# Performance work log

Hardware: AMD Instinct MI355X
Metric: run time of the kernel (lower is better)

The kernel has to match this reference:

```python
import jax, jax.numpy as jnp
import numpy as np

DIM = 128
HEADS = 4
K = 7          # neighborhood kernel size
MLP_RATIO = 4
EPS = 1e-5


def setup_inputs() -> dict:
    key = jax.random.key(0)
    ks = jax.random.split(key, 8)
    B, H, W, C = 4, 64, 64, DIM
    hid = C * MLP_RATIO
    s = lambda k, shape: jax.random.normal(k, shape, jnp.float32) * 0.02
    return {
        "x": jax.random.normal(ks[0], (B, H, W, C), jnp.float32),
        "ln1_g": jnp.ones((C,), jnp.float32),
        "ln1_b": jnp.zeros((C,), jnp.float32),
        "qkv_w": s(ks[1], (C, 3 * C)),
        "qkv_b": jnp.zeros((3 * C,), jnp.float32),
        "rpb": s(ks[2], (HEADS, 2 * K - 1, 2 * K - 1)),
        "proj_w": s(ks[3], (C, C)),
        "proj_b": jnp.zeros((C,), jnp.float32),
        "ln2_g": jnp.ones((C,), jnp.float32),
        "ln2_b": jnp.zeros((C,), jnp.float32),
        "fc1_w": s(ks[4], (C, hid)),
        "fc1_b": jnp.zeros((hid,), jnp.float32),
        "fc2_w": s(ks[5], (hid, C)),
        "fc2_b": jnp.zeros((C,), jnp.float32),
    }


def _ln(x, g, b):
    m = jnp.mean(x, axis=-1, keepdims=True)
    v = jnp.mean(jnp.square(x - m), axis=-1, keepdims=True)
    return (x - m) * jax.lax.rsqrt(v + EPS) * g + b


def _neigh_idx(L, k):
    # NATTEN border-clamped neighborhood: start = clamp(i - k//2, 0, L-k)
    i = jnp.arange(L)
    start = jnp.clip(i - k // 2, 0, L - k)
    idx = start[:, None] + jnp.arange(k)[None, :]        # [L, k] key positions
    rel = idx - i[:, None] + (k - 1)                     # [L, k] rpb indices in [0, 2k-2]
    return idx, rel


def _neighborhood_attention(x, qkv_w, qkv_b, rpb, proj_w, proj_b):
    B, H, W, C = x.shape
    nh, hd = HEADS, C // HEADS
    scale = hd ** -0.5
    qkv = (x @ qkv_w + qkv_b).reshape(B, H, W, 3, nh, hd)
    qkv = qkv.transpose(3, 0, 4, 1, 2, 5)                # [3, B, nh, H, W, hd]
    q, k_, v = qkv[0] * scale, qkv[1], qkv[2]
    ih, rh = _neigh_idx(H, K)
    iw, rw = _neigh_idx(W, K)
    # gather 7x7 neighborhoods: [B, nh, H, K, W, K, hd]
    kg = k_[:, :, ih][:, :, :, :, iw]
    vg = v[:, :, ih][:, :, :, :, iw]
    attn = jnp.einsum('bnywc,bnykxjc->bnyxkj', q, kg)    # [B, nh, H, W, K, K]
    bias = rpb[:, rh][:, :, :, rw]                       # [nh, H, K, W, K]
    attn = attn + bias.transpose(0, 1, 3, 2, 4)[None]
    a = jax.nn.softmax(attn.reshape(B, nh, H, W, K * K), axis=-1)
    a = a.reshape(B, nh, H, W, K, K)
    out = jnp.einsum('bnyxkj,bnykxjc->bnyxc', a, vg)     # [B, nh, H, W, hd]
    out = out.transpose(0, 2, 3, 1, 4).reshape(B, H, W, C)
    return out @ proj_w + proj_b


def reference(x, ln1_g, ln1_b, qkv_w, qkv_b, rpb, proj_w, proj_b,
              ln2_g, ln2_b, fc1_w, fc1_b, fc2_w, fc2_b):
    h = x + _neighborhood_attention(_ln(x, ln1_g, ln1_b), qkv_w, qkv_b, rpb, proj_w, proj_b)
    y = _ln(h, ln2_g, ln2_b)
    y = jax.nn.gelu(y @ fc1_w + fc1_b, approximate=False) @ fc2_w + fc2_b
    return h + y
```

## Files before the change

kernel.cpp:

```cpp
#include <hip/hip_runtime.h>
#include <math.h>

#define TOKS 16384
#define CDIM 128
#define NH 4
#define HD 32
#define HID 512
#define QSCALE 0.17677669529663687f
#define LEPS 1e-5f

typedef const float* fp;
typedef const unsigned short* bfp16;
typedef __attribute__((ext_vector_type(8))) short bf16x8;
typedef __attribute__((ext_vector_type(4))) float f32x4;

__device__ inline unsigned int bfp2(float a, float b) {
    unsigned int ua = __float_as_uint(a); ua = (ua + 0x7FFFu + ((ua >> 16) & 1u)) >> 16;
    unsigned int ub = __float_as_uint(b); ub = (ub + 0x7FFFu + ((ub >> 16) & 1u)) >> 16;
    return ua | (ub << 16);
}
__device__ inline unsigned short bf1(float a) {
    unsigned int u = __float_as_uint(a);
    return (unsigned short)((u + 0x7FFFu + ((u >> 16) & 1u)) >> 16);
}
__device__ inline float lo16(unsigned int u) { return __uint_as_float(u << 16); }
__device__ inline float hi16(unsigned int u) { return __uint_as_float(u & 0xFFFF0000u); }

__global__ __launch_bounds__(256) void kw(fp qw, fp pw, fp f1w, fp f2w,
                                          unsigned short* __restrict__ wt) {
    int e = blockIdx.x * 256 + threadIdx.x;
    float v;
    if (e < 49152)       { int n = e >> 7,  k = e & 127;          v = qw[(size_t)k * 384 + n]; }
    else if (e < 65536)  { int i = e - 49152;  int n = i >> 7, k = i & 127; v = pw[(size_t)k * 128 + n]; }
    else if (e < 131072) { int i = e - 65536;  int n = i >> 7, k = i & 127; v = f1w[(size_t)k * 512 + n]; }
    else                 { int i = e - 131072; int n = i >> 9, k = i & 511; v = f2w[(size_t)k * 128 + n]; }
    wt[e] = bf1(v);
}

__global__ __launch_bounds__(256) void k0_ln(fp x, fp g, fp b, unsigned short* __restrict__ xn) {
    const int t = threadIdx.x;
    const int row = blockIdx.x * 8 + (t >> 5);
    const int l = t & 31;
    const float4 v = *(const float4*)(x + (size_t)row * CDIM + l * 4);
    float s = v.x + v.y + v.z + v.w;
    float q = v.x * v.x + v.y * v.y + v.z * v.z + v.w * v.w;
#pragma unroll
    for (int m = 16; m >= 1; m >>= 1) { s += __shfl_xor(s, m); q += __shfl_xor(q, m); }
    float mu = s * (1.f / 128.f);
    float rs = rsqrtf(q * (1.f / 128.f) - mu * mu + LEPS);
    const float4 gv = *(const float4*)(g + l * 4);
    const float4 bv = *(const float4*)(b + l * 4);
    float a0 = (v.x - mu) * rs * gv.x + bv.x, a1 = (v.y - mu) * rs * gv.y + bv.y;
    float a2 = (v.z - mu) * rs * gv.z + bv.z, a3 = (v.w - mu) * rs * gv.w + bv.w;
    uint2 o; o.x = bfp2(a0, a1); o.y = bfp2(a2, a3);
    *(uint2*)(xn + (size_t)row * CDIM + l * 4) = o;
}


__global__ __launch_bounds__(256) void k1_mfma(bfp16 xn, bfp16 wt0, fp wb,
                                               float* __restrict__ qb,
                                               unsigned short* __restrict__ kvb) {
    __shared__ unsigned int lds[8192];
    const int m0 = blockIdx.x * 64;
    const int nb = blockIdx.y * 64;
    const int tid = threadIdx.x;
#pragma unroll
    for (int i = 0; i < 4; i++) {
        int slot = tid + i * 256;
        int m = slot >> 4, c16 = slot & 15;
        const uint4 v4 = *(const uint4*)(xn + (size_t)(m0 + m) * CDIM + c16 * 8);
        *(uint4*)&lds[m * 64 + (c16 ^ (m & 15)) * 4] = v4;
    }
#pragma unroll
    for (int i = 0; i < 4; i++) {
        int slot = tid + i * 256;
        int n = slot >> 4, c16 = slot & 15;
        const uint4 v4 = *(const uint4*)(wt0 + (size_t)(nb + n) * 128 + c16 * 8);
        *(uint4*)&lds[4096 + n * 64 + (c16 ^ (n & 15)) * 4] = v4;
    }
    __syncthreads();

    const int lane = tid & 63, wid = tid >> 6, quad = lane >> 4, l16 = lane & 15;
    const int mrow = wid * 16 + l16;
    f32x4 acc[4];
#pragma unroll
    for (int nt = 0; nt < 4; nt++) acc[nt] = (f32x4){0.f, 0.f, 0.f, 0.f};
#pragma unroll
    for (int kk = 0; kk < 128; kk += 32) {
        int c = (kk >> 3) + quad;
        bf16x8 a = *(bf16x8*)&lds[mrow * 64 + (c ^ l16) * 4];
#pragma unroll
        for (int nt = 0; nt < 4; nt++) {
            bf16x8 bf = *(bf16x8*)&lds[4096 + (nt * 16 + l16) * 64 + (c ^ l16) * 4];
            acc[nt] = __builtin_amdgcn_mfma_f32_16x16x32_bf16(a, bf, acc[nt], 0, 0, 0);
        }
    }
#pragma unroll
    for (int nt = 0; nt < 4; nt++) {
        int col = nb + nt * 16 + l16;
        float bias = wb[col];
#pragma unroll
        for (int r = 0; r < 4; r++) {
            int row = m0 + wid * 16 + quad * 4 + r;
            float vres = acc[nt][r] + bias;
            if (col < 128)
                qb[(size_t)row * 128 + col] = vres * QSCALE;
            else if (col < 256)
                kvb[(size_t)row * 256 + (col - 128)] = bf1(vres);
            else
                kvb[(size_t)row * 256 + 128 + (col - 256)] = bf1(vres);
        }
    }
}

__global__ __launch_bounds__(256) void k2_attn(const float* __restrict__ qb,
                                               const unsigned short* __restrict__ kvb,
                                               fp rpb, unsigned short* __restrict__ attnb) {
    const int gid = blockIdx.x * 256 + threadIdx.x;
    const int d = gid & 3;
    const int g = (gid >> 2) & 3;
    const int head = (gid >> 4) & 3;
    const int token = gid >> 6;
    const int bb = token >> 12;
    const int y = (token >> 6) & 63;
    const int xx = token & 63;
    const int sy = min(max(y - 3, 0), 57);
    const int sx = min(max(xx - 3, 0), 57);

    const int koff = head * HD + d * 8;
    float q[8];
    {
        const float4* qp = (const float4*)(qb + (size_t)token * 128 + koff);
        float4 q0 = qp[0], q1 = qp[1];
        q[0] = q0.x; q[1] = q0.y; q[2] = q0.z; q[3] = q0.w;
        q[4] = q1.x; q[5] = q1.y; q[6] = q1.z; q[7] = q1.w;
    }

    const float* rp = rpb + head * 169 + (sy - y + 6) * 13 + (sx - xx + 6);
    const int nbase = (bb << 12) + sy * 64 + sx;

    float sc[13];
#pragma unroll
    for (int i = 0; i < 13; i++) {
        int n = g * 13 + i;
        bool ok = n < 49;
        int nn = ok ? n : 48;
        int dy = nn / 7, dx = nn - dy * 7;
        const uint4 kk = *(const uint4*)(kvb + (size_t)(nbase + dy * 64 + dx) * 256 + koff);
        float s = q[0] * lo16(kk.x) + q[1] * hi16(kk.x)
                + q[2] * lo16(kk.y) + q[3] * hi16(kk.y)
                + q[4] * lo16(kk.z) + q[5] * hi16(kk.z)
                + q[6] * lo16(kk.w) + q[7] * hi16(kk.w);
        s += __shfl_xor(s, 1);
        s += __shfl_xor(s, 2);
        sc[i] = ok ? (s + rp[dy * 13 + dx]) : -1e30f;
    }
    float mx = sc[0];
#pragma unroll
    for (int l = 1; l < 13; l++) mx = fmaxf(mx, sc[l]);
    mx = fmaxf(mx, __shfl_xor(mx, 4));
    mx = fmaxf(mx, __shfl_xor(mx, 8));
    float sum = 0.f;
#pragma unroll
    for (int l = 0; l < 13; l++) { sc[l] = __expf(sc[l] - mx); sum += sc[l]; }
    sum += __shfl_xor(sum, 4);
    sum += __shfl_xor(sum, 8);
    float inv = 1.f / sum;

    float o[8];
#pragma unroll
    for (int i = 0; i < 8; i++) o[i] = 0.f;
#pragma unroll
    for (int i = 0; i < 13; i++) {
        int n = g * 13 + i;
        int nn = (n < 49) ? n : 48;
        int dy = nn / 7, dx = nn - dy * 7;
        float p = sc[i] * inv;
        const uint4 vv = *(const uint4*)(kvb + (size_t)(nbase + dy * 64 + dx) * 256 + 128 + koff);
        o[0] += p * lo16(vv.x); o[1] += p * hi16(vv.x);
        o[2] += p * lo16(vv.y); o[3] += p * hi16(vv.y);
        o[4] += p * lo16(vv.z); o[5] += p * hi16(vv.z);
        o[6] += p * lo16(vv.w); o[7] += p * hi16(vv.w);
    }
#pragma unroll
    for (int i = 0; i < 8; i++) {
        o[i] += __shfl_xor(o[i], 4);
        o[i] += __shfl_xor(o[i], 8);
    }
    if (g == 0) {
        uint4 ov;
        ov.x = bfp2(o[0], o[1]); ov.y = bfp2(o[2], o[3]);
        ov.z = bfp2(o[4], o[5]); ov.w = bfp2(o[6], o[7]);
        *(uint4*)(attnb + (size_t)token * 128 + koff) = ov;
    }
}

__global__ __launch_bounds__(256) void k3_mfma(bfp16 attnb, fp x, bfp16 wt1, fp wb,
                                               float* __restrict__ h) {
    __shared__ unsigned int lds[8192];
    const int m0 = blockIdx.x * 64;
    const int nb = blockIdx.y * 64;
    const int tid = threadIdx.x;
#pragma unroll
    for (int i = 0; i < 4; i++) {
        int slot = tid + i * 256;
        int m = slot >> 4, c16 = slot & 15;
        const uint4 v4 = *(const uint4*)(attnb + (size_t)(m0 + m) * 128 + c16 * 8);
        *(uint4*)&lds[m * 64 + (c16 ^ (m & 15)) * 4] = v4;
    }
#pragma unroll
    for (int i = 0; i < 4; i++) {
        int slot = tid + i * 256;
        int n = slot >> 4, c16 = slot & 15;
        const uint4 v4 = *(const uint4*)(wt1 + (size_t)(nb + n) * 128 + c16 * 8);
        *(uint4*)&lds[4096 + n * 64 + (c16 ^ (n & 15)) * 4] = v4;
    }
    __syncthreads();

    const int lane = tid & 63, wid = tid >> 6, quad = lane >> 4, l16 = lane & 15;
    const int mrow = wid * 16 + l16;
    f32x4 acc[4];
#pragma unroll
    for (int nt = 0; nt < 4; nt++) acc[nt] = (f32x4){0.f, 0.f, 0.f, 0.f};
#pragma unroll
    for (int kk = 0; kk < 128; kk += 32) {
        int c = (kk >> 3) + quad;
        bf16x8 a = *(bf16x8*)&lds[mrow * 64 + (c ^ l16) * 4];
#pragma unroll
        for (int nt = 0; nt < 4; nt++) {
            bf16x8 bf = *(bf16x8*)&lds[4096 + (nt * 16 + l16) * 64 + (c ^ l16) * 4];
            acc[nt] = __builtin_amdgcn_mfma_f32_16x16x32_bf16(a, bf, acc[nt], 0, 0, 0);
        }
    }
#pragma unroll
    for (int nt = 0; nt < 4; nt++) {
        int col = nb + nt * 16 + l16;
        float bias = wb[col];
#pragma unroll
        for (int r = 0; r < 4; r++) {
            int row = m0 + wid * 16 + quad * 4 + r;
            h[(size_t)row * CDIM + col] = x[(size_t)row * CDIM + col] + acc[nt][r] + bias;
        }
    }
}

__global__ __launch_bounds__(256) void k4_mfma(bfp16 hn, bfp16 wt2, fp wb,
                                               unsigned short* __restrict__ y1) {
    __shared__ unsigned int lds[8192];
    const int m0 = blockIdx.x * 64;
    const int nb = blockIdx.y * 64;
    const int tid = threadIdx.x;
#pragma unroll
    for (int i = 0; i < 4; i++) {
        int slot = tid + i * 256;
        int m = slot >> 4, c16 = slot & 15;
        const uint4 v4 = *(const uint4*)(hn + (size_t)(m0 + m) * CDIM + c16 * 8);
        *(uint4*)&lds[m * 64 + (c16 ^ (m & 15)) * 4] = v4;
    }
#pragma unroll
    for (int i = 0; i < 4; i++) {
        int slot = tid + i * 256;
        int n = slot >> 4, c16 = slot & 15;
        const uint4 v4 = *(const uint4*)(wt2 + (size_t)(nb + n) * 128 + c16 * 8);
        *(uint4*)&lds[4096 + n * 64 + (c16 ^ (n & 15)) * 4] = v4;
    }
    __syncthreads();

    const int lane = tid & 63, wid = tid >> 6, quad = lane >> 4, l16 = lane & 15;
    const int mrow = wid * 16 + l16;
    f32x4 acc[4];
#pragma unroll
    for (int nt = 0; nt < 4; nt++) acc[nt] = (f32x4){0.f, 0.f, 0.f, 0.f};
#pragma unroll
    for (int kk = 0; kk < 128; kk += 32) {
        int c = (kk >> 3) + quad;
        bf16x8 a = *(bf16x8*)&lds[mrow * 64 + (c ^ l16) * 4];
#pragma unroll
        for (int nt = 0; nt < 4; nt++) {
            bf16x8 bf = *(bf16x8*)&lds[4096 + (nt * 16 + l16) * 64 + (c ^ l16) * 4];
            acc[nt] = __builtin_amdgcn_mfma_f32_16x16x32_bf16(a, bf, acc[nt], 0, 0, 0);
        }
    }
#pragma unroll
    for (int nt = 0; nt < 4; nt++) {
        int col = nb + nt * 16 + l16;
        float bias = wb[col];
#pragma unroll
        for (int r = 0; r < 4; r++) {
            int row = m0 + wid * 16 + quad * 4 + r;
            float z = acc[nt][r] + bias;
            y1[(size_t)row * HID + col] = bf1(0.5f * z * (1.f + erff(z * 0.70710678118654752f)));
        }
    }
}

__global__ __launch_bounds__(256) void k5_mfma(bfp16 y1, fp h, bfp16 wt3, fp wb,
                                               float* __restrict__ out) {
    __shared__ unsigned int lds[8192];
    const int m0 = blockIdx.x * 64;
    const int nb = blockIdx.y * 64;
    const int tid = threadIdx.x;
    const int lane = tid & 63, wid = tid >> 6, quad = lane >> 4, l16 = lane & 15;
    const int mrow = wid * 16 + l16;
    f32x4 acc[4];
#pragma unroll
    for (int nt = 0; nt < 4; nt++) acc[nt] = (f32x4){0.f, 0.f, 0.f, 0.f};

    for (int kc = 0; kc < 4; kc++) {
        if (kc) __syncthreads();
#pragma unroll
        for (int i = 0; i < 4; i++) {
            int slot = tid + i * 256;
            int m = slot >> 4, c16 = slot & 15;
            const uint4 v4 = *(const uint4*)(y1 + (size_t)(m0 + m) * HID + kc * 128 + c16 * 8);
            *(uint4*)&lds[m * 64 + (c16 ^ (m & 15)) * 4] = v4;
        }
#pragma unroll
        for (int i = 0; i < 4; i++) {
            int slot = tid + i * 256;
            int n = slot >> 4, c16 = slot & 15;
            const uint4 v4 = *(const uint4*)(wt3 + (size_t)(nb + n) * 512 + kc * 128 + c16 * 8);
            *(uint4*)&lds[4096 + n * 64 + (c16 ^ (n & 15)) * 4] = v4;
        }
        __syncthreads();
#pragma unroll
        for (int kk = 0; kk < 128; kk += 32) {
            int c = (kk >> 3) + quad;
            bf16x8 a = *(bf16x8*)&lds[mrow * 64 + (c ^ l16) * 4];
#pragma unroll
            for (int nt = 0; nt < 4; nt++) {
                bf16x8 bf = *(bf16x8*)&lds[4096 + (nt * 16 + l16) * 64 + (c ^ l16) * 4];
                acc[nt] = __builtin_amdgcn_mfma_f32_16x16x32_bf16(a, bf, acc[nt], 0, 0, 0);
            }
        }
    }
#pragma unroll
    for (int nt = 0; nt < 4; nt++) {
        int col = nb + nt * 16 + l16;
        float bias = wb[col];
#pragma unroll
        for (int r = 0; r < 4; r++) {
            int row = m0 + wid * 16 + quad * 4 + r;
            out[(size_t)row * CDIM + col] = h[(size_t)row * CDIM + col] + acc[nt][r] + bias;
        }
    }
}

extern "C" void kernel_launch(void* const* d_in, const int* in_sizes, int n_in,
                              void* d_out, int out_size, void* d_ws, size_t ws_size,
                              hipStream_t stream) {
    fp x      = (fp)d_in[0];
    fp ln1_g  = (fp)d_in[1];
    fp ln1_b  = (fp)d_in[2];
    fp qkv_w  = (fp)d_in[3];
    fp qkv_b  = (fp)d_in[4];
    fp rpb    = (fp)d_in[5];
    fp proj_w = (fp)d_in[6];
    fp proj_b = (fp)d_in[7];
    fp ln2_g  = (fp)d_in[8];
    fp ln2_b  = (fp)d_in[9];
    fp fc1_w  = (fp)d_in[10];
    fp fc1_b  = (fp)d_in[11];
    fp fc2_w  = (fp)d_in[12];
    fp fc2_b  = (fp)d_in[13];
    float* out = (float*)d_out;

    float* ws = (float*)d_ws;
    float* h  = ws;
    unsigned short* xn = (unsigned short*)(h + (size_t)TOKS * CDIM);
    unsigned short* hn = xn + (size_t)TOKS * CDIM;
    float* qb = (float*)(hn + (size_t)TOKS * CDIM);
    unsigned short* kvb   = (unsigned short*)(qb + (size_t)TOKS * CDIM);
    unsigned short* attnb = kvb + (size_t)TOKS * 256;
    unsigned short* wt    = attnb + (size_t)TOKS * CDIM;
    unsigned short* y1    = (unsigned short*)qb;

    unsigned short* wt0 = wt;
    unsigned short* wt1 = wt + 49152;
    unsigned short* wt2 = wt + 65536;
    unsigned short* wt3 = wt + 131072;

    kw<<<768, 256, 0, stream>>>(qkv_w, proj_w, fc1_w, fc2_w, wt);
    k0_ln<<<TOKS / 8, 256, 0, stream>>>(x, ln1_g, ln1_b, xn);
    k1_mfma<<<dim3(TOKS / 64, 6), 256, 0, stream>>>(xn, wt0, qkv_b, qb, kvb);
    k2_attn<<<TOKS * NH * 16 / 256, 256, 0, stream>>>(qb, kvb, rpb, attnb);
    k3_mfma<<<dim3(TOKS / 64, 2), 256, 0, stream>>>(attnb, x, wt1, proj_b, h);
    k0_ln<<<TOKS / 8, 256, 0, stream>>>(h, ln2_g, ln2_b, hn);
    k4_mfma<<<dim3(TOKS / 64, 8), 256, 0, stream>>>(hn, wt2, fc1_b, y1);
    k5_mfma<<<dim3(TOKS / 64, 2), 256, 0, stream>>>(y1, h, fc2_w == nullptr ? wt3 : wt3, fc2_b, out);
}
```

Baseline: 150.5 us.

## Fuse LN2 into proj GEMM, merge prep kernels, enlarge GEMM M-tiles

```diff
diff --git a/kernel.cpp b/kernel.cpp
--- a/kernel.cpp
+++ b/kernel.cpp
@@ -26,46 +26,49 @@
 __device__ inline float lo16(unsigned int u) { return __uint_as_float(u << 16); }
 __device__ inline float hi16(unsigned int u) { return __uint_as_float(u & 0xFFFF0000u); }
 
-__global__ __launch_bounds__(256) void kw(fp qw, fp pw, fp f1w, fp f2w,
-                                          unsigned short* __restrict__ wt) {
-    int e = blockIdx.x * 256 + threadIdx.x;
-    float v;
-    if (e < 49152)       { int n = e >> 7,  k = e & 127;          v = qw[(size_t)k * 384 + n]; }
-    else if (e < 65536)  { int i = e - 49152;  int n = i >> 7, k = i & 127; v = pw[(size_t)k * 128 + n]; }
-    else if (e < 131072) { int i = e - 65536;  int n = i >> 7, k = i & 127; v = f1w[(size_t)k * 512 + n]; }
-    else                 { int i = e - 131072; int n = i >> 9, k = i & 511; v = f2w[(size_t)k * 128 + n]; }
-    wt[e] = bf1(v);
-}
-
-__global__ __launch_bounds__(256) void k0_ln(fp x, fp g, fp b, unsigned short* __restrict__ xn) {
-    const int t = threadIdx.x;
-    const int row = blockIdx.x * 8 + (t >> 5);
-    const int l = t & 31;
-    const float4 v = *(const float4*)(x + (size_t)row * CDIM + l * 4);
-    float s = v.x + v.y + v.z + v.w;
-    float q = v.x * v.x + v.y * v.y + v.z * v.z + v.w * v.w;
-#pragma unroll
-    for (int m = 16; m >= 1; m >>= 1) { s += __shfl_xor(s, m); q += __shfl_xor(q, m); }
-    float mu = s * (1.f / 128.f);
-    float rs = rsqrtf(q * (1.f / 128.f) - mu * mu + LEPS);
-    const float4 gv = *(const float4*)(g + l * 4);
-    const float4 bv = *(const float4*)(b + l * 4);
-    float a0 = (v.x - mu) * rs * gv.x + bv.x, a1 = (v.y - mu) * rs * gv.y + bv.y;
-    float a2 = (v.z - mu) * rs * gv.z + bv.z, a3 = (v.w - mu) * rs * gv.w + bv.w;
-    uint2 o; o.x = bfp2(a0, a1); o.y = bfp2(a2, a3);
-    *(uint2*)(xn + (size_t)row * CDIM + l * 4) = o;
+__global__ __launch_bounds__(256) void prep(fp qw, fp pw, fp f1w, fp f2w,
+                                            fp x, fp g, fp b,
+                                            unsigned short* __restrict__ wt,
+                                            unsigned short* __restrict__ xn) {
+    const int bid = blockIdx.x;
+    if (bid < 768) {
+        int e = bid * 256 + threadIdx.x;
+        float v;
+        if (e < 49152)       { int n = e >> 7,  k = e & 127;          v = qw[(size_t)k * 384 + n]; }
+        else if (e < 65536)  { int i = e - 49152;  int n = i >> 7, k = i & 127; v = pw[(size_t)k * 128 + n]; }
+        else if (e < 131072) { int i = e - 65536;  int n = i >> 7, k = i & 127; v = f1w[(size_t)k * 512 + n]; }
+        else                 { int i = e - 131072; int n = i >> 9, k = i & 511; v = f2w[(size_t)k * 128 + n]; }
+        wt[e] = bf1(v);
+    } else {
+        const int t = threadIdx.x;
+        const int row = (bid - 768) * 8 + (t >> 5);
+        const int l = t & 31;
+        const float4 v = *(const float4*)(x + (size_t)row * CDIM + l * 4);
+        float s = v.x + v.y + v.z + v.w;
+        float q = v.x * v.x + v.y * v.y + v.z * v.z + v.w * v.w;
+#pragma unroll
+        for (int m = 16; m >= 1; m >>= 1) { s += __shfl_xor(s, m); q += __shfl_xor(q, m); }
+        float mu = s * (1.f / 128.f);
+        float rs = rsqrtf(q * (1.f / 128.f) - mu * mu + LEPS);
+        const float4 gv = *(const float4*)(g + l * 4);
+        const float4 bv = *(const float4*)(b + l * 4);
+        float a0 = (v.x - mu) * rs * gv.x + bv.x, a1 = (v.y - mu) * rs * gv.y + bv.y;
+        float a2 = (v.z - mu) * rs * gv.z + bv.z, a3 = (v.w - mu) * rs * gv.w + bv.w;
+        uint2 o; o.x = bfp2(a0, a1); o.y = bfp2(a2, a3);
+        *(uint2*)(xn + (size_t)row * CDIM + l * 4) = o;
+    }
 }
 
 
 __global__ __launch_bounds__(256) void k1_mfma(bfp16 xn, bfp16 wt0, fp wb,
                                                float* __restrict__ qb,
                                                unsigned short* __restrict__ kvb) {
-    __shared__ unsigned int lds[8192];
-    const int m0 = blockIdx.x * 64;
+    __shared__ unsigned int lds[12288];
+    const int m0 = blockIdx.x * 128;
     const int nb = blockIdx.y * 64;
     const int tid = threadIdx.x;
 #pragma unroll
-    for (int i = 0; i < 4; i++) {
+    for (int i = 0; i < 8; i++) {
         int slot = tid + i * 256;
         int m = slot >> 4, c16 = slot & 15;
         const uint4 v4 = *(const uint4*)(xn + (size_t)(m0 + m) * CDIM + c16 * 8);
@@ -76,23 +79,26 @@
         int slot = tid + i * 256;
         int n = slot >> 4, c16 = slot & 15;
         const uint4 v4 = *(const uint4*)(wt0 + (size_t)(nb + n) * 128 + c16 * 8);
-        *(uint4*)&lds[4096 + n * 64 + (c16 ^ (n & 15)) * 4] = v4;
+        *(uint4*)&lds[8192 + n * 64 + (c16 ^ (n & 15)) * 4] = v4;
     }
     __syncthreads();
 
     const int lane = tid & 63, wid = tid >> 6, quad = lane >> 4, l16 = lane & 15;
-    const int mrow = wid * 16 + l16;
-    f32x4 acc[4];
-#pragma unroll
-    for (int nt = 0; nt < 4; nt++) acc[nt] = (f32x4){0.f, 0.f, 0.f, 0.f};
-#pragma unroll
-    for (int kk = 0; kk < 128; kk += 32) {
-        int c = (kk >> 3) + quad;
-        bf16x8 a = *(bf16x8*)&lds[mrow * 64 + (c ^ l16) * 4];
+    f32x4 acc[2][4];
+#pragma unroll
+    for (int mt = 0; mt < 2; mt++)
+#pragma unroll
+        for (int nt = 0; nt < 4; nt++) acc[mt][nt] = (f32x4){0.f, 0.f, 0.f, 0.f};
+#pragma unroll
+    for (int kk = 0; kk < 4; kk++) {
+        int c = kk * 4 + quad;
+        bf16x8 a0 = *(bf16x8*)&lds[(wid * 32 + l16) * 64 + (c ^ l16) * 4];
+        bf16x8 a1 = *(bf16x8*)&lds[(wid * 32 + 16 + l16) * 64 + (c ^ l16) * 4];
 #pragma unroll
         for (int nt = 0; nt < 4; nt++) {
-            bf16x8 bf = *(bf16x8*)&lds[4096 + (nt * 16 + l16) * 64 + (c ^ l16) * 4];
-            acc[nt] = __builtin_amdgcn_mfma_f32_16x16x32_bf16(a, bf, acc[nt], 0, 0, 0);
+            bf16x8 bf = *(bf16x8*)&lds[8192 + (nt * 16 + l16) * 64 + (c ^ l16) * 4];
+            acc[0][nt] = __builtin_amdgcn_mfma_f32_16x16x32_bf16(a0, bf, acc[0][nt], 0, 0, 0);
+            acc[1][nt] = __builtin_amdgcn_mfma_f32_16x16x32_bf16(a1, bf, acc[1][nt], 0, 0, 0);
         }
     }
 #pragma unroll
@@ -100,16 +106,18 @@
         int col = nb + nt * 16 + l16;
         float bias = wb[col];
 #pragma unroll
-        for (int r = 0; r < 4; r++) {
-            int row = m0 + wid * 16 + quad * 4 + r;
-            float vres = acc[nt][r] + bias;
-            if (col < 128)
-                qb[(size_t)row * 128 + col] = vres * QSCALE;
-            else if (col < 256)
-                kvb[(size_t)row * 256 + (col - 128)] = bf1(vres);
-            else
-                kvb[(size_t)row * 256 + 128 + (col - 256)] = bf1(vres);
-        }
+        for (int mt = 0; mt < 2; mt++)
+#pragma unroll
+            for (int r = 0; r < 4; r++) {
+                int row = m0 + wid * 32 + mt * 16 + quad * 4 + r;
+                float vres = acc[mt][nt][r] + bias;
+                if (col < 128)
+                    qb[(size_t)row * 128 + col] = vres * QSCALE;
+                else if (col < 256)
+                    kvb[(size_t)row * 256 + (col - 128)] = bf1(vres);
+                else
+                    kvb[(size_t)row * 256 + 128 + (col - 256)] = bf1(vres);
+            }
     }
 }
 
@@ -195,41 +203,122 @@
     }
 }
 
-__global__ __launch_bounds__(256) void k3_mfma(bfp16 attnb, fp x, bfp16 wt1, fp wb,
-                                               float* __restrict__ h) {
-    __shared__ unsigned int lds[8192];
+__global__ __launch_bounds__(256) void k3_mfma(bfp16 attnb, fp x, bfp16 wt1, fp pb,
+                                               fp g2, fp b2,
+                                               float* __restrict__ h,
+                                               unsigned short* __restrict__ hn) {
+    __shared__ unsigned int lds[12288];
     const int m0 = blockIdx.x * 64;
+    const int tid = threadIdx.x;
+#pragma unroll
+    for (int i = 0; i < 4; i++) {
+        int slot = tid + i * 256;
+        int m = slot >> 4, c16 = slot & 15;
+        const uint4 v4 = *(const uint4*)(attnb + (size_t)(m0 + m) * CDIM + c16 * 8);
+        *(uint4*)&lds[m * 64 + (c16 ^ (m & 15)) * 4] = v4;
+    }
+#pragma unroll
+    for (int i = 0; i < 8; i++) {
+        int slot = tid + i * 256;
+        int n = slot >> 4, c16 = slot & 15;
+        const uint4 v4 = *(const uint4*)(wt1 + (size_t)n * 128 + c16 * 8);
+        *(uint4*)&lds[4096 + n * 64 + (c16 ^ (n & 15)) * 4] = v4;
+    }
+    __syncthreads();
+
+    const int lane = tid & 63, wid = tid >> 6, quad = lane >> 4, l16 = lane & 15;
+    const int mrow = wid * 16 + l16;
+    f32x4 acc[8];
+#pragma unroll
+    for (int nt = 0; nt < 8; nt++) acc[nt] = (f32x4){0.f, 0.f, 0.f, 0.f};
+#pragma unroll
+    for (int kk = 0; kk < 4; kk++) {
+        int c = kk * 4 + quad;
+        bf16x8 a = *(bf16x8*)&lds[mrow * 64 + (c ^ l16) * 4];
+#pragma unroll
+        for (int nt = 0; nt < 8; nt++) {
+            bf16x8 bf = *(bf16x8*)&lds[4096 + (nt * 16 + l16) * 64 + (c ^ l16) * 4];
+            acc[nt] = __builtin_amdgcn_mfma_f32_16x16x32_bf16(a, bf, acc[nt], 0, 0, 0);
+        }
+    }
+    float s[4] = {0.f, 0.f, 0.f, 0.f}, q[4] = {0.f, 0.f, 0.f, 0.f};
+#pragma unroll
+    for (int nt = 0; nt < 8; nt++) {
+        int col = nt * 16 + l16;
+        float bias = pb[col];
+#pragma unroll
+        for (int r = 0; r < 4; r++) {
+            int row = m0 + wid * 16 + quad * 4 + r;
+            float hv = x[(size_t)row * CDIM + col] + acc[nt][r] + bias;
+            h[(size_t)row * CDIM + col] = hv;
+            acc[nt][r] = hv;
+            s[r] += hv; q[r] += hv * hv;
+        }
+    }
+#pragma unroll
+    for (int m = 1; m <= 8; m <<= 1) {
+#pragma unroll
+        for (int r = 0; r < 4; r++) {
+            s[r] += __shfl_xor(s[r], m);
+            q[r] += __shfl_xor(q[r], m);
+        }
+    }
+    float mu[4], rs[4];
+#pragma unroll
+    for (int r = 0; r < 4; r++) {
+        mu[r] = s[r] * (1.f / 128.f);
+        rs[r] = rsqrtf(q[r] * (1.f / 128.f) - mu[r] * mu[r] + LEPS);
+    }
+#pragma unroll
+    for (int nt = 0; nt < 8; nt++) {
+        int col = nt * 16 + l16;
+        float gg = g2[col], bb = b2[col];
+#pragma unroll
+        for (int r = 0; r < 4; r++) {
+            int row = m0 + wid * 16 + quad * 4 + r;
+            hn[(size_t)row * CDIM + col] = bf1((acc[nt][r] - mu[r]) * rs[r] * gg + bb);
+        }
+    }
+}
+
+__global__ __launch_bounds__(256) void k4_mfma(bfp16 hn, bfp16 wt2, fp wb,
+                                               unsigned short* __restrict__ y1) {
+    __shared__ unsigned int lds[12288];
+    const int m0 = blockIdx.x * 128;
     const int nb = blockIdx.y * 64;
     const int tid = threadIdx.x;
 #pragma unroll
+    for (int i = 0; i < 8; i++) {
+        int slot = tid + i * 256;
+        int m = slot >> 4, c16 = slot & 15;
+        const uint4 v4 = *(const uint4*)(hn + (size_t)(m0 + m) * CDIM + c16 * 8);
+        *(uint4*)&lds[m * 64 + (c16 ^ (m & 15)) * 4] = v4;
+    }
+#pragma unroll
     for (int i = 0; i < 4; i++) {
         int slot = tid + i * 256;
-        int m = slot >> 4, c16 = slot & 15;
-        const uint4 v4 = *(const uint4*)(attnb + (size_t)(m0 + m) * 128 + c16 * 8);
-        *(uint4*)&lds[m * 64 + (c16 ^ (m & 15)) * 4] = v4;
-    }
-#pragma unroll
-    for (int i = 0; i < 4; i++) {
-        int slot = tid + i * 256;
         int n = slot >> 4, c16 = slot & 15;
-        const uint4 v4 = *(const uint4*)(wt1 + (size_t)(nb + n) * 128 + c16 * 8);
-        *(uint4*)&lds[4096 + n * 64 + (c16 ^ (n & 15)) * 4] = v4;
+        const uint4 v4 = *(const uint4*)(wt2 + (size_t)(nb + n) * 128 + c16 * 8);
+        *(uint4*)&lds[8192 + n * 64 + (c16 ^ (n & 15)) * 4] = v4;
     }
     __syncthreads();
 
     const int lane = tid & 63, wid = tid >> 6, quad = lane >> 4, l16 = lane & 15;
-    const int mrow = wid * 16 + l16;
-    f32x4 acc[4];
-#pragma unroll
-    for (int nt = 0; nt < 4; nt++) acc[nt] = (f32x4){0.f, 0.f, 0.f, 0.f};
-#pragma unroll
-    for (int kk = 0; kk < 128; kk += 32) {
-        int c = (kk >> 3) + quad;
-        bf16x8 a = *(bf16x8*)&lds[mrow * 64 + (c ^ l16) * 4];
+    f32x4 acc[2][4];
+#pragma unroll
+    for (int mt = 0; mt < 2; mt++)
+#pragma unroll
+        for (int nt = 0; nt < 4; nt++) acc[mt][nt] = (f32x4){0.f, 0.f, 0.f, 0.f};
+#pragma unroll
+    for (int kk = 0; kk < 4; kk++) {
+        int c = kk * 4 + quad;
+        bf16x8 a0 = *(bf16x8*)&lds[(wid * 32 + l16) * 64 + (c ^ l16) * 4];
+        bf16x8 a1 = *(bf16x8*)&lds[(wid * 32 + 16 + l16) * 64 + (c ^ l16) * 4];
 #pragma unroll
         for (int nt = 0; nt < 4; nt++) {
-            bf16x8 bf = *(bf16x8*)&lds[4096 + (nt * 16 + l16) * 64 + (c ^ l16) * 4];
-            acc[nt] = __builtin_amdgcn_mfma_f32_16x16x32_bf16(a, bf, acc[nt], 0, 0, 0);
+            bf16x8 bf = *(bf16x8*)&lds[8192 + (nt * 16 + l16) * 64 + (c ^ l16) * 4];
+            acc[0][nt] = __builtin_amdgcn_mfma_f32_16x16x32_bf16(a0, bf, acc[0][nt], 0, 0, 0);
+            acc[1][nt] = __builtin_amdgcn_mfma_f32_16x16x32_bf16(a1, bf, acc[1][nt], 0, 0, 0);
         }
     }
 #pragma unroll
@@ -237,79 +326,33 @@
         int col = nb + nt * 16 + l16;
         float bias = wb[col];
 #pragma unroll
-        for (int r = 0; r < 4; r++) {
-            int row = m0 + wid * 16 + quad * 4 + r;
-            h[(size_t)row * CDIM + col] = x[(size_t)row * CDIM + col] + acc[nt][r] + bias;
-        }
-    }
-}
-
-__global__ __launch_bounds__(256) void k4_mfma(bfp16 hn, bfp16 wt2, fp wb,
-                                               unsigned short* __restrict__ y1) {
-    __shared__ unsigned int lds[8192];
-    const int m0 = blockIdx.x * 64;
-    const int nb = blockIdx.y * 64;
-    const int tid = threadIdx.x;
-#pragma unroll
-    for (int i = 0; i < 4; i++) {
-        int slot = tid + i * 256;
-        int m = slot >> 4, c16 = slot & 15;
-        const uint4 v4 = *(const uint4*)(hn + (size_t)(m0 + m) * CDIM + c16 * 8);
-        *(uint4*)&lds[m * 64 + (c16 ^ (m & 15)) * 4] = v4;
-    }
-#pragma unroll
-    for (int i = 0; i < 4; i++) {
-        int slot = tid + i * 256;
-        int n = slot >> 4, c16 = slot & 15;
-        const uint4 v4 = *(const uint4*)(wt2 + (size_t)(nb + n) * 128 + c16 * 8);
-        *(uint4*)&lds[4096 + n * 64 + (c16 ^ (n & 15)) * 4] = v4;
-    }
-    __syncthreads();
-
-    const int lane = tid & 63, wid = tid >> 6, quad = lane >> 4, l16 = lane & 15;
-    const int mrow = wid * 16 + l16;
-    f32x4 acc[4];
-#pragma unroll
-    for (int nt = 0; nt < 4; nt++) acc[nt] = (f32x4){0.f, 0.f, 0.f, 0.f};
-#pragma unroll
-    for (int kk = 0; kk < 128; kk += 32) {
-        int c = (kk >> 3) + quad;
-        bf16x8 a = *(bf16x8*)&lds[mrow * 64 + (c ^ l16) * 4];
-#pragma unroll
-        for (int nt = 0; nt < 4; nt++) {
-            bf16x8 bf = *(bf16x8*)&lds[4096 + (nt * 16 + l16) * 64 + (c ^ l16) * 4];
-            acc[nt] = __builtin_amdgcn_mfma_f32_16x16x32_bf16(a, bf, acc[nt], 0, 0, 0);
-        }
-    }
-#pragma unroll
-    for (int nt = 0; nt < 4; nt++) {
-        int col = nb + nt * 16 + l16;
-        float bias = wb[col];
-#pragma unroll
-        for (int r = 0; r < 4; r++) {
-            int row = m0 + wid * 16 + quad * 4 + r;
-            float z = acc[nt][r] + bias;
-            y1[(size_t)row * HID + col] = bf1(0.5f * z * (1.f + erff(z * 0.70710678118654752f)));
-        }
+        for (int mt = 0; mt < 2; mt++)
+#pragma unroll
+            for (int r = 0; r < 4; r++) {
+                int row = m0 + wid * 32 + mt * 16 + quad * 4 + r;
+                float z = acc[mt][nt][r] + bias;
+                y1[(size_t)row * HID + col] = bf1(0.5f * z * (1.f + erff(z * 0.70710678118654752f)));
+            }
     }
 }
 
 __global__ __launch_bounds__(256) void k5_mfma(bfp16 y1, fp h, bfp16 wt3, fp wb,
                                                float* __restrict__ out) {
-    __shared__ unsigned int lds[8192];
-    const int m0 = blockIdx.x * 64;
+    __shared__ unsigned int lds[12288];
+    const int m0 = blockIdx.x * 128;
     const int nb = blockIdx.y * 64;
     const int tid = threadIdx.x;
     const int lane = tid & 63, wid = tid >> 6, quad = lane >> 4, l16 = lane & 15;
-    const int mrow = wid * 16 + l16;
-    f32x4 acc[4];
-#pragma unroll
-    for (int nt = 0; nt < 4; nt++) acc[nt] = (f32x4){0.f, 0.f, 0.f, 0.f};
+    f32x4 acc[2][4];
+#pragma unroll
+    for (int mt = 0; mt < 2; mt++)
+#pragma unroll
+        for (int nt = 0; nt < 4; nt++) acc[mt][nt] = (f32x4){0.f, 0.f, 0.f, 0.f};
 
     for (int kc = 0; kc < 4; kc++) {
         if (kc) __syncthreads();
 #pragma unroll
-        for (int i = 0; i < 4; i++) {
+        for (int i = 0; i < 8; i++) {
             int slot = tid + i * 256;
             int m = slot >> 4, c16 = slot & 15;
             const uint4 v4 = *(const uint4*)(y1 + (size_t)(m0 + m) * HID + kc * 128 + c16 * 8);
@@ -320,17 +363,19 @@
             int slot = tid + i * 256;
             int n = slot >> 4, c16 = slot & 15;
             const uint4 v4 = *(const uint4*)(wt3 + (size_t)(nb + n) * 512 + kc * 128 + c16 * 8);
-            *(uint4*)&lds[4096 + n * 64 + (c16 ^ (n & 15)) * 4] = v4;
+            *(uint4*)&lds[8192 + n * 64 + (c16 ^ (n & 15)) * 4] = v4;
         }
         __syncthreads();
 #pragma unroll
-        for (int kk = 0; kk < 128; kk += 32) {
-            int c = (kk >> 3) + quad;
-            bf16x8 a = *(bf16x8*)&lds[mrow * 64 + (c ^ l16) * 4];
+        for (int kk = 0; kk < 4; kk++) {
+            int c = kk * 4 + quad;
+            bf16x8 a0 = *(bf16x8*)&lds[(wid * 32 + l16) * 64 + (c ^ l16) * 4];
+            bf16x8 a1 = *(bf16x8*)&lds[(wid * 32 + 16 + l16) * 64 + (c ^ l16) * 4];
 #pragma unroll
             for (int nt = 0; nt < 4; nt++) {
-                bf16x8 bf = *(bf16x8*)&lds[4096 + (nt * 16 + l16) * 64 + (c ^ l16) * 4];
-                acc[nt] = __builtin_amdgcn_mfma_f32_16x16x32_bf16(a, bf, acc[nt], 0, 0, 0);
+                bf16x8 bf = *(bf16x8*)&lds[8192 + (nt * 16 + l16) * 64 + (c ^ l16) * 4];
+                acc[0][nt] = __builtin_amdgcn_mfma_f32_16x16x32_bf16(a0, bf, acc[0][nt], 0, 0, 0);
+                acc[1][nt] = __builtin_amdgcn_mfma_f32_16x16x32_bf16(a1, bf, acc[1][nt], 0, 0, 0);
             }
         }
     }
@@ -339,10 +384,12 @@
         int col = nb + nt * 16 + l16;
         float bias = wb[col];
 #pragma unroll
-        for (int r = 0; r < 4; r++) {
-            int row = m0 + wid * 16 + quad * 4 + r;
-            out[(size_t)row * CDIM + col] = h[(size_t)row * CDIM + col] + acc[nt][r] + bias;
-        }
+        for (int mt = 0; mt < 2; mt++)
+#pragma unroll
+            for (int r = 0; r < 4; r++) {
+                int row = m0 + wid * 32 + mt * 16 + quad * 4 + r;
+                out[(size_t)row * CDIM + col] = h[(size_t)row * CDIM + col] + acc[mt][nt][r] + bias;
+            }
     }
 }
 
@@ -380,12 +427,10 @@
     unsigned short* wt2 = wt + 65536;
     unsigned short* wt3 = wt + 131072;
 
-    kw<<<768, 256, 0, stream>>>(qkv_w, proj_w, fc1_w, fc2_w, wt);
-    k0_ln<<<TOKS / 8, 256, 0, stream>>>(x, ln1_g, ln1_b, xn);
-    k1_mfma<<<dim3(TOKS / 64, 6), 256, 0, stream>>>(xn, wt0, qkv_b, qb, kvb);
+    prep<<<768 + TOKS / 8, 256, 0, stream>>>(qkv_w, proj_w, fc1_w, fc2_w, x, ln1_g, ln1_b, wt, xn);
+    k1_mfma<<<dim3(TOKS / 128, 6), 256, 0, stream>>>(xn, wt0, qkv_b, qb, kvb);
     k2_attn<<<TOKS * NH * 16 / 256, 256, 0, stream>>>(qb, kvb, rpb, attnb);
-    k3_mfma<<<dim3(TOKS / 64, 2), 256, 0, stream>>>(attnb, x, wt1, proj_b, h);
-    k0_ln<<<TOKS / 8, 256, 0, stream>>>(h, ln2_g, ln2_b, hn);
-    k4_mfma<<<dim3(TOKS / 64, 8), 256, 0, stream>>>(hn, wt2, fc1_b, y1);
-    k5_mfma<<<dim3(TOKS / 64, 2), 256, 0, stream>>>(y1, h, fc2_w == nullptr ? wt3 : wt3, fc2_b, out);
-}
+    k3_mfma<<<TOKS / 64, 256, 0, stream>>>(attnb, x, wt1, proj_b, ln2_g, ln2_b, h, hn);
+    k4_mfma<<<dim3(TOKS / 128, 8), 256, 0, stream>>>(hn, wt2, fc1_b, y1);
+    k5_mfma<<<dim3(TOKS / 128, 2), 256, 0, stream>>>(y1, h, wt3, fc2_b, out);
+}
```

After: 149.3 us (median of 2 runs). Within noise of the previous version (-0.8%).
